# Performance work log

Measured on AMD Instinct MI355X. Metric: run time of the kernel, lower is better.

## Reference

```python
import jax, jax.numpy as jnp
import numpy as np

EPS = 1e-07


def _center_to_corner(box):
    # box: [N,4] (cx, cy, w, h) -> [N,4] (x1, y1, x2, y2)
    cx, cy, w, h = box[:, 0], box[:, 1], box[:, 2], box[:, 3]
    return jnp.stack([cx - w / 2, cy - h / 2, cx + w / 2, cy + h / 2], axis=1)


def setup_inputs() -> dict:
    key = jax.random.key(0)
    k1, k2 = jax.random.split(key)
    N = 8192
    pred_boxes = jax.random.uniform(k1, (N, 4), dtype=jnp.float32)
    target_boxes = jax.random.uniform(k2, (N, 4), dtype=jnp.float32)
    return {"pred_boxes": pred_boxes, "target_boxes": target_boxes}


def reference(pred_boxes, target_boxes):
    # Faithful to the original: full [N,N] pairwise IoU matrix, then diagonal.
    b1 = _center_to_corner(pred_boxes)   # [N,4]
    b2 = _center_to_corner(target_boxes)  # [N,4]

    inter_x1 = jnp.maximum(b1[:, 0:1], b2[None, :, 0])  # [N,N]
    inter_y1 = jnp.maximum(b1[:, 1:2], b2[None, :, 1])
    inter_x2 = jnp.minimum(b1[:, 2:3], b2[None, :, 2])
    inter_y2 = jnp.minimum(b1[:, 3:4], b2[None, :, 3])

    inter_area = jnp.clip(inter_x2 - inter_x1, 0.0) * jnp.clip(inter_y2 - inter_y1, 0.0)

    area1 = (b1[:, 2] - b1[:, 0]) * (b1[:, 3] - b1[:, 1])  # [N]
    area2 = (b2[:, 2] - b2[:, 0]) * (b2[:, 3] - b2[:, 1])  # [N]
    union_area = area1[:, None] + area2[None, :] - inter_area  # [N,N]

    iou = inter_area / (union_area + EPS)  # [N,N]
    loss = 1.0 - jnp.diagonal(iou)         # [N]
    return loss.mean()
```

## Files before the change

kernel.cpp:

```cpp
#include <hip/hip_runtime.h>

#define EPS_IOU 1e-7f

__global__ __launch_bounds__(1024) void IoULoss_75213467287779_kernel(
    const float4* __restrict__ pred, const float4* __restrict__ targ,
    float* __restrict__ out, int n) {
    const int tid = threadIdx.x;
    float sum = 0.0f;
    #pragma unroll
    for (int k = 0; k < 8; ++k) {
        int i = tid + k * 1024;
        if (i < n) {
            float4 p = pred[i];
            float4 t = targ[i];
            float px1 = p.x - p.z * 0.5f, px2 = p.x + p.z * 0.5f;
            float py1 = p.y - p.w * 0.5f, py2 = p.y + p.w * 0.5f;
            float tx1 = t.x - t.z * 0.5f, tx2 = t.x + t.z * 0.5f;
            float ty1 = t.y - t.w * 0.5f, ty2 = t.y + t.w * 0.5f;

            float ix = fminf(px2, tx2) - fmaxf(px1, tx1);
            float iy = fminf(py2, ty2) - fmaxf(py1, ty1);
            float inter = fmaxf(ix, 0.0f) * fmaxf(iy, 0.0f);

            float a1 = (px2 - px1) * (py2 - py1);
            float a2 = (tx2 - tx1) * (ty2 - ty1);
            float uni = a1 + a2 - inter;
            sum += inter / (uni + EPS_IOU);
        }
    }

    #pragma unroll
    for (int off = 32; off > 0; off >>= 1)
        sum += __shfl_down(sum, off, 64);

    __shared__ float wsum[16];
    const int wid = tid >> 6;
    const int lane = tid & 63;
    if (lane == 0) wsum[wid] = sum;
    __syncthreads();

    if (wid == 0) {
        float s = (lane < 16) ? wsum[lane] : 0.0f;
        #pragma unroll
        for (int off = 8; off > 0; off >>= 1)
            s += __shfl_down(s, off, 64);
        if (lane == 0) out[0] = 1.0f - s / (float)n;
    }
}

extern "C" void kernel_launch(void* const* d_in, const int* in_sizes, int n_in,
                              void* d_out, int out_size, void* d_ws, size_t ws_size,
                              hipStream_t stream) {
    const float4* pred = (const float4*)d_in[0];
    const float4* targ = (const float4*)d_in[1];
    float* out = (float*)d_out;
    const int n = in_sizes[0] / 4;
    IoULoss_75213467287779_kernel<<<1, 1024, 0, stream>>>(pred, targ, out, n);
}
```

Baseline: 10.51 us.

## Split IoU loss into multi-block partial sums plus a final reduction kernel

Replaces the single 1024-thread block with a grid of 256-thread blocks, one box pair per thread, each writing a partial sum to workspace. A second 64-thread kernel reduces the partials and writes the loss. This spreads the loads across many compute units instead of one, at the cost of an extra kernel launch and a workspace round-trip. The final kernel only handles up to 64 partial sums, which is enough for N=8192 (32 blocks) but would drop partials for larger N.

```diff
diff --git a/kernel.cpp b/kernel.cpp
--- a/kernel.cpp
+++ b/kernel.cpp
@@ -2,50 +2,52 @@
 
 #define EPS_IOU 1e-7f
 
-__global__ __launch_bounds__(1024) void IoULoss_75213467287779_kernel(
+__global__ __launch_bounds__(256) void iou_partial_kernel(
     const float4* __restrict__ pred, const float4* __restrict__ targ,
-    float* __restrict__ out, int n) {
-    const int tid = threadIdx.x;
+    float* __restrict__ ws, int n) {
+    const int i = blockIdx.x * 256 + threadIdx.x;
     float sum = 0.0f;
-    #pragma unroll
-    for (int k = 0; k < 8; ++k) {
-        int i = tid + k * 1024;
-        if (i < n) {
-            float4 p = pred[i];
-            float4 t = targ[i];
-            float px1 = p.x - p.z * 0.5f, px2 = p.x + p.z * 0.5f;
-            float py1 = p.y - p.w * 0.5f, py2 = p.y + p.w * 0.5f;
-            float tx1 = t.x - t.z * 0.5f, tx2 = t.x + t.z * 0.5f;
-            float ty1 = t.y - t.w * 0.5f, ty2 = t.y + t.w * 0.5f;
+    if (i < n) {
+        float4 p = pred[i];
+        float4 t = targ[i];
+        float px1 = p.x - p.z * 0.5f, px2 = p.x + p.z * 0.5f;
+        float py1 = p.y - p.w * 0.5f, py2 = p.y + p.w * 0.5f;
+        float tx1 = t.x - t.z * 0.5f, tx2 = t.x + t.z * 0.5f;
+        float ty1 = t.y - t.w * 0.5f, ty2 = t.y + t.w * 0.5f;
 
-            float ix = fminf(px2, tx2) - fmaxf(px1, tx1);
-            float iy = fminf(py2, ty2) - fmaxf(py1, ty1);
-            float inter = fmaxf(ix, 0.0f) * fmaxf(iy, 0.0f);
+        float ix = fminf(px2, tx2) - fmaxf(px1, tx1);
+        float iy = fminf(py2, ty2) - fmaxf(py1, ty1);
+        float inter = fmaxf(ix, 0.0f) * fmaxf(iy, 0.0f);
 
-            float a1 = (px2 - px1) * (py2 - py1);
-            float a2 = (tx2 - tx1) * (ty2 - ty1);
-            float uni = a1 + a2 - inter;
-            sum += inter / (uni + EPS_IOU);
-        }
+        float a1 = (px2 - px1) * (py2 - py1);
+        float a2 = (tx2 - tx1) * (ty2 - ty1);
+        float uni = a1 + a2 - inter;
+        sum = inter / (uni + EPS_IOU);
     }
 
     #pragma unroll
     for (int off = 32; off > 0; off >>= 1)
         sum += __shfl_down(sum, off, 64);
 
-    __shared__ float wsum[16];
-    const int wid = tid >> 6;
-    const int lane = tid & 63;
+    __shared__ float wsum[4];
+    const int wid = threadIdx.x >> 6;
+    const int lane = threadIdx.x & 63;
     if (lane == 0) wsum[wid] = sum;
     __syncthreads();
 
-    if (wid == 0) {
-        float s = (lane < 16) ? wsum[lane] : 0.0f;
-        #pragma unroll
-        for (int off = 8; off > 0; off >>= 1)
-            s += __shfl_down(s, off, 64);
-        if (lane == 0) out[0] = 1.0f - s / (float)n;
-    }
+    if (threadIdx.x == 0)
+        ws[blockIdx.x] = wsum[0] + wsum[1] + wsum[2] + wsum[3];
+}
+
+__global__ __launch_bounds__(64) void iou_final_kernel(
+    const float* __restrict__ ws, float* __restrict__ out,
+    int nblocks, int n) {
+    const int lane = threadIdx.x;
+    float s = (lane < nblocks) ? ws[lane] : 0.0f;
+    #pragma unroll
+    for (int off = 32; off > 0; off >>= 1)
+        s += __shfl_down(s, off, 64);
+    if (lane == 0) out[0] = 1.0f - s / (float)n;
 }
 
 extern "C" void kernel_launch(void* const* d_in, const int* in_sizes, int n_in,
@@ -54,6 +56,9 @@
     const float4* pred = (const float4*)d_in[0];
     const float4* targ = (const float4*)d_in[1];
     float* out = (float*)d_out;
+    float* ws = (float*)d_ws;
     const int n = in_sizes[0] / 4;
-    IoULoss_75213467287779_kernel<<<1, 1024, 0, stream>>>(pred, targ, out, n);
+    const int nblocks = (n + 255) / 256;
+    iou_partial_kernel<<<nblocks, 256, 0, stream>>>(pred, targ, ws, n);
+    iou_final_kernel<<<1, 64, 0, stream>>>(ws, out, nblocks, n);
 }
```

New measurement: 10.87 us. 3.4% more time.
